# Kernel tuning notes

Measured on AMD Instinct MI355X. Metric: run time of the kernel, lower is better.

Reference implementation:

```python
import jax, jax.numpy as jnp
import numpy as np

N_NOTE = 14  # undefined global in original; must equal output_size for one-hot feedback


def setup_inputs() -> dict:
    key = jax.random.key(0)
    ks = jax.random.split(key, 9)
    B, T, H, O = 256, 512, 2048, 14
    s_i = 1.0 / np.sqrt(14)
    s_h = 1.0 / np.sqrt(H)
    return {
        "encoder_outputs": jax.random.normal(ks[0], (B, 1, H), jnp.float32),
        "encoder_hidden": jax.random.normal(ks[1], (1, B, H), jnp.float32),
        "target_tensor": jax.random.uniform(ks[2], (B, T, O), jnp.float32),
        "W_ih": jax.random.normal(ks[3], (3 * H, 14), jnp.float32) * s_i,
        "W_hh": jax.random.normal(ks[4], (3 * H, H), jnp.float32) * s_h,
        "b_ih": jax.random.normal(ks[5], (3 * H,), jnp.float32) * s_h,
        "b_hh": jax.random.normal(ks[6], (3 * H,), jnp.float32) * s_h,
        "W_out": jax.random.normal(ks[7], (O, H), jnp.float32) * s_h,
        "b_out": jax.random.normal(ks[8], (O,), jnp.float32) * s_h,
    }


def _decode(encoder_hidden, target_tensor, W_ih, W_hh, b_ih, b_hh, W_out, b_out):
    B, T, O = target_tensor.shape
    H = W_hh.shape[1]

    def step(carry, _):
        h, x = carry  # h: [B,H], x: [B,14]
        xr = jax.nn.relu(x)
        gi = xr @ W_ih.T + b_ih            # [B,3H]
        gh = h @ W_hh.T + b_hh             # [B,3H]
        r = jax.nn.sigmoid(gi[:, :H] + gh[:, :H])
        z = jax.nn.sigmoid(gi[:, H:2 * H] + gh[:, H:2 * H])
        n = jnp.tanh(gi[:, 2 * H:] + r * gh[:, 2 * H:])
        h_new = (1.0 - z) * n + z * h
        logits = h_new @ W_out.T + b_out   # [B,O]
        # feedback: one-hot of argmax; the Python `break` in the original zeros
        # every batch element at-or-after the first hit of n_note-1
        topi = jnp.argmax(logits, axis=-1)                     # [B]
        hit = (topi == N_NOTE - 1).astype(jnp.int32)
        alive = (jnp.cumsum(hit) == 0).astype(logits.dtype)    # inclusive cumsum
        x_next = jax.nn.one_hot(topi, O, dtype=logits.dtype) * alive[:, None]
        return (h_new, x_next), logits

    h0 = encoder_hidden[0]          # [B,H]
    x0 = target_tensor[:, 0]        # [B,14] first-step input
    (h_final, _), logits = jax.lax.scan(step, (h0, x0), None, length=T)
    logits = jnp.transpose(logits, (1, 0, 2))  # [B,T,O]
    log_probs = jax.nn.log_softmax(logits, axis=-1)
    return log_probs, h_final[None]  # ([B,T,O], [1,B,H])


def reference(encoder_outputs, encoder_hidden, target_tensor, W_ih, W_hh, b_ih, b_hh, W_out, b_out):
    # encoder_outputs is accepted but unused, matching the original forward
    return _decode(encoder_hidden, target_tensor, W_ih, W_hh, b_ih, b_hh, W_out, b_out)
```

## Files before the change

kernel.cpp:

```cpp
#include <hip/hip_runtime.h>
#include <math.h>

typedef float f4 __attribute__((ext_vector_type(4)));
typedef _Float16 f16x8 __attribute__((ext_vector_type(8)));
typedef _Float16 f16x4 __attribute__((ext_vector_type(4)));
typedef int i4 __attribute__((ext_vector_type(4)));

#define Hdim 2048
#define Bdim 256
#define Tdim 512
#define Odim 14
#define G3   6144


__global__ void prep_gtable(const float* __restrict__ b_ih,
                            const float* __restrict__ W_ih,
                            float* __restrict__ Gt) {
    int idx = blockIdx.x * 256 + threadIdx.x;
    if (idx >= 15 * G3) return;
    int c = idx / G3, row = idx % G3;
    float v = b_ih[row];
    if (c < Odim) v += W_ih[row * Odim + c];
    Gt[idx] = v;
}

__global__ void prep_gi0(const float* __restrict__ b_ih,
                         const float* __restrict__ W_ih,
                         const float* __restrict__ target,
                         float* __restrict__ gi0) {
    int idx = blockIdx.x * 256 + threadIdx.x;
    int b = idx / G3, row = idx % G3;
    const float* x0 = target + (size_t)b * (Tdim * Odim);
    float s = b_ih[row];
    #pragma unroll
    for (int c = 0; c < Odim; ++c)
        s = fmaf(fmaxf(x0[c], 0.f), W_ih[row * Odim + c], s);
    gi0[idx] = s;
}

__global__ void prep_Bpack(const float* __restrict__ W,
                           _Float16* __restrict__ Bh, _Float16* __restrict__ Bl) {
    int idx = blockIdx.x * 256 + threadIdx.x;
    int n = idx >> 8, kc = idx & 255;
    const float* src = W + (size_t)n * Hdim + kc * 8;
    int kb = kc >> 2, q = kc & 3;
    int lane = (n & 15) + 16 * q;
    int nt = n >> 4;
    f16x8 vh, vl;
    #pragma unroll
    for (int j = 0; j < 8; ++j) {
        float w = src[j];
        _Float16 h = (_Float16)w;
        vh[j] = h;
        vl[j] = (_Float16)(w - (float)h);
    }
    size_t off = (((size_t)nt * 64 + kb) * 64 + lane) * 8;
    *(f16x8*)(Bh + off) = vh;
    *(f16x8*)(Bl + off) = vl;
}

__global__ void prep_A0(const float* __restrict__ h0,
                        _Float16* __restrict__ Ah, _Float16* __restrict__ Al) {
    int idx = blockIdx.x * 256 + threadIdx.x;
    int m = idx >> 8, kc = idx & 255;
    const float* src = h0 + (size_t)m * Hdim + kc * 8;
    int kb = kc >> 2, q = kc & 3;
    int lane = (m & 15) + 16 * q;
    int mt = m >> 4;
    f16x8 vh, vl;
    #pragma unroll
    for (int j = 0; j < 8; ++j) {
        float w = src[j];
        _Float16 h = (_Float16)w;
        vh[j] = h;
        vl[j] = (_Float16)(w - (float)h);
    }
    size_t off = (((size_t)mt * 64 + kb) * 64 + lane) * 8;
    *(f16x8*)(Ah + off) = vh;
    *(f16x8*)(Al + off) = vl;
}

__global__ __launch_bounds__(512, 4)
void gemm_step(const _Float16* __restrict__ Ah, const _Float16* __restrict__ Al,
               const _Float16* __restrict__ Bh, const _Float16* __restrict__ Bl,
               float* __restrict__ Cpart) {
    __shared__ __align__(16) _Float16 sB[2][12288];

    const int tid = threadIdx.x;
    const int wave = tid >> 6, lane = tid & 63;
    const int nt0 = blockIdx.x * 3;
    const int kb0 = blockIdx.y * 16;

    f4 acc[2][3];
    #pragma unroll
    for (int mf = 0; mf < 2; ++mf)
        #pragma unroll
        for (int nf = 0; nf < 3; ++nf) acc[mf][nf] = (f4)0.f;

    auto stage = [&](int buf, int c) {
        #pragma unroll
        for (int i = 0; i < 3; ++i) {
            int e = i * 512 + tid;
            int half = (e >= 768) ? 1 : 0;
            int r = e - half * 768;
            int blk = r >> 6, l = e & 63;
            int ntl = blk >> 2, kbl = blk & 3;
            const _Float16* src = (half ? Bl : Bh) +
                ((((size_t)(nt0 + ntl) * 64) + kb0 + c * 4 + kbl) * 512 + l * 8);
            __builtin_amdgcn_global_load_lds(
                (const __attribute__((address_space(1))) void*)src,
                (__attribute__((address_space(3))) void*)(&sB[buf][(size_t)e * 8]),
                16, 0, 0);
        }
    };

    stage(0, 0);
    __syncthreads();

    for (int c = 0; c < 4; ++c) {
        const int buf = c & 1;
        if (c < 3) stage(buf ^ 1, c + 1);
        #pragma unroll
        for (int kbl = 0; kbl < 4; ++kbl) {
            const int kb = kb0 + c * 4 + kbl;
            f16x8 a_h[2], a_l[2], b_h[3], b_l[3];
            #pragma unroll
            for (int mf = 0; mf < 2; ++mf) {
                size_t off = (((size_t)(wave * 2 + mf) * 64 + kb) * 64 + lane) * 8;
                a_h[mf] = *(const f16x8*)(Ah + off);
                a_l[mf] = *(const f16x8*)(Al + off);
            }
            #pragma unroll
            for (int nf = 0; nf < 3; ++nf) {
                int base = ((nf * 4 + kbl) * 64 + lane) * 8;
                b_h[nf] = *(const f16x8*)(&sB[buf][base]);
                b_l[nf] = *(const f16x8*)(&sB[buf][6144 + base]);
            }
            #pragma unroll
            for (int mf = 0; mf < 2; ++mf)
                #pragma unroll
                for (int nf = 0; nf < 3; ++nf) {
                    acc[mf][nf] = __builtin_amdgcn_mfma_f32_16x16x32_f16(
                        a_h[mf], b_h[nf], acc[mf][nf], 0, 0, 0);
                    acc[mf][nf] = __builtin_amdgcn_mfma_f32_16x16x32_f16(
                        a_h[mf], b_l[nf], acc[mf][nf], 0, 0, 0);
                    acc[mf][nf] = __builtin_amdgcn_mfma_f32_16x16x32_f16(
                        a_l[mf], b_h[nf], acc[mf][nf], 0, 0, 0);
                }
        }
        __syncthreads();
    }

    const size_t base = (size_t)blockIdx.y * Bdim * G3;
    #pragma unroll
    for (int mf = 0; mf < 2; ++mf) {
        int mrow = wave * 32 + mf * 16 + (lane >> 4) * 4;
        #pragma unroll
        for (int nf = 0; nf < 3; ++nf) {
            int n = (nt0 + nf) * 16 + (lane & 15);
            #pragma unroll
            for (int q = 0; q < 4; ++q)
                Cpart[base + (size_t)(mrow + q) * G3 + n] = acc[mf][nf][q];
        }
    }
}

__global__ __launch_bounds__(512)
void fused_out(const float* __restrict__ hprev, float* __restrict__ hnew,
               const float* __restrict__ Cpart, const float* __restrict__ Gt,
               const float* __restrict__ gi0, const float* __restrict__ b_hh,
               const float* __restrict__ W_out, const float* __restrict__ b_out,
               _Float16* __restrict__ Ah, _Float16* __restrict__ Al,
               const int* __restrict__ topi_in, int* __restrict__ topi_out,
               float* __restrict__ lp, float* __restrict__ hfin, int t) {
    const int b = blockIdx.x;
    const int tid = threadIdx.x;
    __shared__ __align__(16) float sh[Hdim];
    __shared__ float sl[16];
    __shared__ int s_sel;
    __shared__ unsigned long long s_m[4];

    if (t > 0) {
        if (tid < 256) {
            int tp = topi_in[tid];
            unsigned long long m = __ballot(tp == (Odim - 1));
            if ((tid & 63) == 0) s_m[tid >> 6] = m;
        }
        __syncthreads();
        if (tid == 0) {
            int bw = b >> 6, bl = b & 63;
            unsigned long long le =
                s_m[bw] & ((bl == 63) ? ~0ULL : ((1ULL << (bl + 1)) - 1ULL));
            bool dead = (le != 0ULL);
            for (int w = 0; w < bw; ++w) dead = dead || (s_m[w] != 0ULL);
            s_sel = dead ? Odim : topi_in[b];
        }
        __syncthreads();
    }
    const float* gp = (t == 0) ? (gi0 + (size_t)b * G3)
                               : (Gt + (size_t)s_sel * G3);

    const int j0 = tid * 4;
    float hn[4];
    {
        float gsum[3][4];
        #pragma unroll
        for (int g = 0; g < 3; ++g) {
            f4 s = *(const f4*)(b_hh + g * Hdim + j0);
            #pragma unroll
            for (int ks = 0; ks < 4; ++ks)
                s += *(const f4*)(Cpart + ((size_t)ks * Bdim + b) * G3 + g * Hdim + j0);
            #pragma unroll
            for (int c = 0; c < 4; ++c) gsum[g][c] = s[c];
        }
        f4 hp = *(const f4*)(hprev + (size_t)b * Hdim + j0);
        f4 gr = *(const f4*)(gp + j0);
        f4 gz = *(const f4*)(gp + Hdim + j0);
        f4 gn = *(const f4*)(gp + 2 * Hdim + j0);
        #pragma unroll
        for (int c = 0; c < 4; ++c) {
            float rr = 1.f / (1.f + expf(-(gr[c] + gsum[0][c])));
            float zz = 1.f / (1.f + expf(-(gz[c] + gsum[1][c])));
            float nn = tanhf(fmaf(rr, gsum[2][c], gn[c]));
            hn[c] = (1.f - zz) * nn + zz * hp[c];
        }
    }
    f4 o0;
    #pragma unroll
    for (int c = 0; c < 4; ++c) o0[c] = hn[c];
    *(f4*)(hnew + (size_t)b * Hdim + j0) = o0;
    {
        f16x4 vh, vl;
        #pragma unroll
        for (int c = 0; c < 4; ++c) {
            _Float16 hh = (_Float16)hn[c];
            vh[c] = hh;
            vl[c] = (_Float16)(hn[c] - (float)hh);
        }
        int kb = j0 >> 5, q = (j0 >> 3) & 3, e0 = j0 & 7;
        int lane = (b & 15) + 16 * q, mt = b >> 4;
        size_t off = (((size_t)mt * 64 + kb) * 64 + lane) * 8 + e0;
        *(f16x4*)(Ah + off) = vh;
        *(f16x4*)(Al + off) = vl;
    }
    *(f4*)(sh + j0) = o0;
    __syncthreads();

    const int w = tid >> 6, l = tid & 63;
    for (int o = w; o < Odim; o += 8) {
        const float* wo = W_out + (size_t)o * Hdim;
        float s = 0.f;
        #pragma unroll
        for (int i = 0; i < 32; ++i)
            s = fmaf(sh[l + 64 * i], wo[l + 64 * i], s);
        #pragma unroll
        for (int off = 32; off >= 1; off >>= 1)
            s += __shfl_down(s, off);
        if (l == 0) sl[o] = s + b_out[o];
    }
    __syncthreads();
    if (tid == 0) {
        float m = sl[0]; int bi = 0;
        #pragma unroll
        for (int o = 1; o < Odim; ++o)
            if (sl[o] > m) { m = sl[o]; bi = o; }
        float ssum = 0.f;
        #pragma unroll
        for (int o = 0; o < Odim; ++o) ssum += expf(sl[o] - m);
        topi_out[b] = bi;
        sl[14] = m + logf(ssum);
    }
    __syncthreads();
    if (tid < Odim)
        lp[(size_t)b * (Tdim * Odim) + (size_t)t * Odim + tid] = sl[tid] - sl[14];
    if (hfin)
        *(f4*)(hfin + (size_t)b * Hdim + j0) = o0;
}

extern "C" void kernel_launch(void* const* d_in, const int* in_sizes, int n_in,
                              void* d_out, int out_size, void* d_ws, size_t ws_size,
                              hipStream_t stream) {
    const float* enc_hidden = (const float*)d_in[1];
    const float* target     = (const float*)d_in[2];
    const float* W_ih       = (const float*)d_in[3];
    const float* W_hh       = (const float*)d_in[4];
    const float* b_ih       = (const float*)d_in[5];
    const float* b_hh       = (const float*)d_in[6];
    const float* W_out      = (const float*)d_in[7];
    const float* b_out      = (const float*)d_in[8];

    float* out  = (float*)d_out;
    float* lp   = out;
    float* hfin = out + (size_t)Bdim * Tdim * Odim;

    float* ws    = (float*)d_ws;
    float* hb0   = ws;
    float* hb1   = hb0 + 524288;
    float* Gt    = hb1 + 524288;
    float* gi0   = Gt + 15 * G3;
    float* Cpart = gi0 + (size_t)Bdim * G3;
    _Float16* Ah = (_Float16*)(Cpart + 4 * (size_t)Bdim * G3);
    _Float16* Al = Ah + (size_t)Bdim * Hdim;
    _Float16* Bh = Al + (size_t)Bdim * Hdim;
    _Float16* Bl = Bh + (size_t)G3 * Hdim;
    int* topibuf = (int*)(Bl + (size_t)G3 * Hdim);

    prep_gtable<<<(15 * G3 + 255) / 256, 256, 0, stream>>>(b_ih, W_ih, Gt);
    prep_gi0<<<(Bdim * G3) / 256, 256, 0, stream>>>(b_ih, W_ih, target, gi0);
    prep_Bpack<<<(G3 * 256) / 256, 256, 0, stream>>>(W_hh, Bh, Bl);
    prep_A0<<<(Bdim * 256) / 256, 256, 0, stream>>>(enc_hidden, Ah, Al);

    for (int t = 0; t < Tdim; ++t) {
        float* hnew = (t & 1) ? hb1 : hb0;
        const float* hprev = (t == 0) ? enc_hidden : ((t & 1) ? hb0 : hb1);
        int* tin  = topibuf + ((t + 1) & 1) * 256;
        int* tout = topibuf + (t & 1) * 256;
        gemm_step<<<dim3(128, 4), 512, 0, stream>>>(Ah, Al, Bh, Bl, Cpart);
        fused_out<<<256, 512, 0, stream>>>(hprev, hnew, Cpart, Gt, gi0, b_hh,
                                           W_out, b_out, Ah, Al, tin, tout, lp,
                                           (t == Tdim - 1) ? hfin : nullptr, t);
    }
}
```

Baseline: 18.87 ms.

## Switch per-step GEMM to 32x32x16 MFMA tiles with larger block tiles

```diff
diff --git a/kernel.cpp b/kernel.cpp
--- a/kernel.cpp
+++ b/kernel.cpp
@@ -2,6 +2,7 @@
 #include <math.h>
 
 typedef float f4 __attribute__((ext_vector_type(4)));
+typedef float f16f __attribute__((ext_vector_type(16)));
 typedef _Float16 f16x8 __attribute__((ext_vector_type(8)));
 typedef _Float16 f16x4 __attribute__((ext_vector_type(4)));
 typedef int i4 __attribute__((ext_vector_type(4)));
@@ -43,9 +44,9 @@
     int idx = blockIdx.x * 256 + threadIdx.x;
     int n = idx >> 8, kc = idx & 255;
     const float* src = W + (size_t)n * Hdim + kc * 8;
-    int kb = kc >> 2, q = kc & 3;
-    int lane = (n & 15) + 16 * q;
-    int nt = n >> 4;
+    int kb = kc >> 1;
+    int lane = (n & 31) + 32 * (kc & 1);
+    int nt = n >> 5;
     f16x8 vh, vl;
     #pragma unroll
     for (int j = 0; j < 8; ++j) {
@@ -54,7 +55,7 @@
         vh[j] = h;
         vl[j] = (_Float16)(w - (float)h);
     }
-    size_t off = (((size_t)nt * 64 + kb) * 64 + lane) * 8;
+    size_t off = (((size_t)nt * 128 + kb) * 64 + lane) * 8;
     *(f16x8*)(Bh + off) = vh;
     *(f16x8*)(Bl + off) = vl;
 }
@@ -64,9 +65,9 @@
     int idx = blockIdx.x * 256 + threadIdx.x;
     int m = idx >> 8, kc = idx & 255;
     const float* src = h0 + (size_t)m * Hdim + kc * 8;
-    int kb = kc >> 2, q = kc & 3;
-    int lane = (m & 15) + 16 * q;
-    int mt = m >> 4;
+    int kb = kc >> 1;
+    int lane = (m & 31) + 32 * (kc & 1);
+    int mt = m >> 5;
     f16x8 vh, vl;
     #pragma unroll
     for (int j = 0; j < 8; ++j) {
@@ -75,38 +76,41 @@
         vh[j] = h;
         vl[j] = (_Float16)(w - (float)h);
     }
-    size_t off = (((size_t)mt * 64 + kb) * 64 + lane) * 8;
+    size_t off = (((size_t)mt * 128 + kb) * 64 + lane) * 8;
     *(f16x8*)(Ah + off) = vh;
     *(f16x8*)(Al + off) = vl;
 }
 
-__global__ __launch_bounds__(512, 4)
+__global__ __launch_bounds__(256, 1)
 void gemm_step(const _Float16* __restrict__ Ah, const _Float16* __restrict__ Al,
                const _Float16* __restrict__ Bh, const _Float16* __restrict__ Bl,
                float* __restrict__ Cpart) {
-    __shared__ __align__(16) _Float16 sB[2][12288];
+    __shared__ __align__(16) _Float16 sB[2][24576];
 
     const int tid = threadIdx.x;
     const int wave = tid >> 6, lane = tid & 63;
-    const int nt0 = blockIdx.x * 3;
-    const int kb0 = blockIdx.y * 16;
-
-    f4 acc[2][3];
+    const int Mg = wave & 1;
+    const int Ng = wave >> 1;
+    const int mb = blockIdx.x & 1;
+    const int nb = blockIdx.x >> 1;
+    const int kb0 = blockIdx.y * 32;
+
+    f16f acc[2][3];
     #pragma unroll
     for (int mf = 0; mf < 2; ++mf)
         #pragma unroll
-        for (int nf = 0; nf < 3; ++nf) acc[mf][nf] = (f4)0.f;
+        for (int nf = 0; nf < 3; ++nf) acc[mf][nf] = (f16f)0.f;
 
     auto stage = [&](int buf, int c) {
         #pragma unroll
-        for (int i = 0; i < 3; ++i) {
-            int e = i * 512 + tid;
-            int half = (e >= 768) ? 1 : 0;
-            int r = e - half * 768;
+        for (int i = 0; i < 12; ++i) {
+            int e = i * 256 + tid;
+            int half = (e >= 1536) ? 1 : 0;
+            int r = e - half * 1536;
             int blk = r >> 6, l = e & 63;
-            int ntl = blk >> 2, kbl = blk & 3;
+            int ntl = blk >> 2, kl = blk & 3;
             const _Float16* src = (half ? Bl : Bh) +
-                ((((size_t)(nt0 + ntl) * 64) + kb0 + c * 4 + kbl) * 512 + l * 8);
+                ((((size_t)(nb * 6 + ntl) * 128) + kb0 + c * 4 + kl) * 512 + l * 8);
             __builtin_amdgcn_global_load_lds(
                 (const __attribute__((address_space(1))) void*)src,
                 (__attribute__((address_space(3))) void*)(&sB[buf][(size_t)e * 8]),
@@ -117,34 +121,35 @@
     stage(0, 0);
     __syncthreads();
 
-    for (int c = 0; c < 4; ++c) {
+    for (int c = 0; c < 8; ++c) {
         const int buf = c & 1;
-        if (c < 3) stage(buf ^ 1, c + 1);
-        #pragma unroll
-        for (int kbl = 0; kbl < 4; ++kbl) {
-            const int kb = kb0 + c * 4 + kbl;
+        if (c < 7) stage(buf ^ 1, c + 1);
+        #pragma unroll
+        for (int kl = 0; kl < 4; ++kl) {
+            const int kb = kb0 + c * 4 + kl;
             f16x8 a_h[2], a_l[2], b_h[3], b_l[3];
             #pragma unroll
             for (int mf = 0; mf < 2; ++mf) {
-                size_t off = (((size_t)(wave * 2 + mf) * 64 + kb) * 64 + lane) * 8;
+                int mt = mb * 4 + Mg * 2 + mf;
+                size_t off = (((size_t)mt * 128 + kb) * 64 + lane) * 8;
                 a_h[mf] = *(const f16x8*)(Ah + off);
                 a_l[mf] = *(const f16x8*)(Al + off);
             }
             #pragma unroll
             for (int nf = 0; nf < 3; ++nf) {
-                int base = ((nf * 4 + kbl) * 64 + lane) * 8;
+                int base = (((Ng * 3 + nf) * 4 + kl) * 64 + lane) * 8;
                 b_h[nf] = *(const f16x8*)(&sB[buf][base]);
-                b_l[nf] = *(const f16x8*)(&sB[buf][6144 + base]);
+                b_l[nf] = *(const f16x8*)(&sB[buf][12288 + base]);
             }
             #pragma unroll
             for (int mf = 0; mf < 2; ++mf)
                 #pragma unroll
                 for (int nf = 0; nf < 3; ++nf) {
-                    acc[mf][nf] = __builtin_amdgcn_mfma_f32_16x16x32_f16(
+                    acc[mf][nf] = __builtin_amdgcn_mfma_f32_32x32x16_f16(
                         a_h[mf], b_h[nf], acc[mf][nf], 0, 0, 0);
-                    acc[mf][nf] = __builtin_amdgcn_mfma_f32_16x16x32_f16(
+                    acc[mf][nf] = __builtin_amdgcn_mfma_f32_32x32x16_f16(
                         a_h[mf], b_l[nf], acc[mf][nf], 0, 0, 0);
-                    acc[mf][nf] = __builtin_amdgcn_mfma_f32_16x16x32_f16(
+                    acc[mf][nf] = __builtin_amdgcn_mfma_f32_32x32x16_f16(
                         a_l[mf], b_h[nf], acc[mf][nf], 0, 0, 0);
                 }
         }
@@ -152,15 +157,18 @@
     }
 
     const size_t base = (size_t)blockIdx.y * Bdim * G3;
+    const int rbase = 4 * (lane >> 5);
     #pragma unroll
     for (int mf = 0; mf < 2; ++mf) {
-        int mrow = wave * 32 + mf * 16 + (lane >> 4) * 4;
+        int m0 = mb * 128 + Mg * 64 + mf * 32 + rbase;
         #pragma unroll
         for (int nf = 0; nf < 3; ++nf) {
-            int n = (nt0 + nf) * 16 + (lane & 15);
+            int n = nb * 192 + (Ng * 3 + nf) * 32 + (lane & 31);
             #pragma unroll
-            for (int q = 0; q < 4; ++q)
-                Cpart[base + (size_t)(mrow + q) * G3 + n] = acc[mf][nf][q];
+            for (int q = 0; q < 16; ++q) {
+                int m = m0 + (q & 3) + 8 * (q >> 2);
+                Cpart[base + (size_t)m * G3 + n] = acc[mf][nf][q];
+            }
         }
     }
 }
@@ -180,6 +188,20 @@
     __shared__ int s_sel;
     __shared__ unsigned long long s_m[4];
 
+    const int j0 = tid * 4;
+
+    float gsum[3][4];
+    #pragma unroll
+    for (int g = 0; g < 3; ++g) {
+        f4 s = *(const f4*)(b_hh + g * Hdim + j0);
+        #pragma unroll
+        for (int ks = 0; ks < 4; ++ks)
+            s += *(const f4*)(Cpart + ((size_t)ks * Bdim + b) * G3 + g * Hdim + j0);
+        #pragma unroll
+        for (int c = 0; c < 4; ++c) gsum[g][c] = s[c];
+    }
+    f4 hp = *(const f4*)(hprev + (size_t)b * Hdim + j0);
+
     if (t > 0) {
         if (tid < 256) {
             int tp = topi_in[tid];
@@ -200,20 +222,8 @@
     const float* gp = (t == 0) ? (gi0 + (size_t)b * G3)
                                : (Gt + (size_t)s_sel * G3);
 
-    const int j0 = tid * 4;
     float hn[4];
     {
-        float gsum[3][4];
-        #pragma unroll
-        for (int g = 0; g < 3; ++g) {
-            f4 s = *(const f4*)(b_hh + g * Hdim + j0);
-            #pragma unroll
-            for (int ks = 0; ks < 4; ++ks)
-                s += *(const f4*)(Cpart + ((size_t)ks * Bdim + b) * G3 + g * Hdim + j0);
-            #pragma unroll
-            for (int c = 0; c < 4; ++c) gsum[g][c] = s[c];
-        }
-        f4 hp = *(const f4*)(hprev + (size_t)b * Hdim + j0);
         f4 gr = *(const f4*)(gp + j0);
         f4 gz = *(const f4*)(gp + Hdim + j0);
         f4 gn = *(const f4*)(gp + 2 * Hdim + j0);
@@ -237,9 +247,9 @@
             vh[c] = hh;
             vl[c] = (_Float16)(hn[c] - (float)hh);
         }
-        int kb = j0 >> 5, q = (j0 >> 3) & 3, e0 = j0 & 7;
-        int lane = (b & 15) + 16 * q, mt = b >> 4;
-        size_t off = (((size_t)mt * 64 + kb) * 64 + lane) * 8 + e0;
+        int kb = j0 >> 4, half = (j0 >> 3) & 1, e0 = j0 & 7;
+        int lane = (b & 31) + 32 * half, mt = b >> 5;
+        size_t off = (((size_t)mt * 128 + kb) * 64 + lane) * 8 + e0;
         *(f16x4*)(Ah + off) = vh;
         *(f16x4*)(Al + off) = vl;
     }
@@ -315,7 +325,7 @@
         const float* hprev = (t == 0) ? enc_hidden : ((t & 1) ? hb0 : hb1);
         int* tin  = topibuf + ((t + 1) & 1) * 256;
         int* tout = topibuf + (t & 1) * 256;
-        gemm_step<<<dim3(128, 4), 512, 0, stream>>>(Ah, Al, Bh, Bl, Cpart);
+        gemm_step<<<dim3(64, 4), 256, 0, stream>>>(Ah, Al, Bh, Bl, Cpart);
         fused_out<<<256, 512, 0, stream>>>(hprev, hnew, Cpart, Gt, gi0, b_hh,
                                            W_out, b_out, Ah, Al, tin, tout, lp,
                                            (t == Tdim - 1) ? hfin : nullptr, t);
```

Result: slower. 22.27 ms (+18.0%).

## Fuse GRU gate epilogue into GEMM with in-block split-K reduction

Applied to the files above, without the earlier changes.

```diff
diff --git a/kernel.cpp b/kernel.cpp
--- a/kernel.cpp
+++ b/kernel.cpp
@@ -3,8 +3,6 @@
 
 typedef float f4 __attribute__((ext_vector_type(4)));
 typedef _Float16 f16x8 __attribute__((ext_vector_type(8)));
-typedef _Float16 f16x4 __attribute__((ext_vector_type(4)));
-typedef int i4 __attribute__((ext_vector_type(4)));
 
 #define Hdim 2048
 #define Bdim 256
@@ -80,16 +78,32 @@
     *(f16x8*)(Al + off) = vl;
 }
 
-__global__ __launch_bounds__(512, 4)
-void gemm_step(const _Float16* __restrict__ Ah, const _Float16* __restrict__ Al,
-               const _Float16* __restrict__ Bh, const _Float16* __restrict__ Bl,
-               float* __restrict__ Cpart) {
-    __shared__ __align__(16) _Float16 sB[2][12288];
+__global__ __launch_bounds__(512, 2)
+void gru_step(const _Float16* __restrict__ Aih, const _Float16* __restrict__ Ail,
+              const _Float16* __restrict__ Bh, const _Float16* __restrict__ Bl,
+              const float* __restrict__ hprev, float* __restrict__ hnew,
+              const float* __restrict__ Gt, const float* __restrict__ gi0,
+              const float* __restrict__ b_hh,
+              const int* __restrict__ topi_in,
+              _Float16* __restrict__ Aoh, _Float16* __restrict__ Aol,
+              int t) {
+    __shared__ __align__(16) _Float16 sB[2][24576];
+    __shared__ unsigned long long s_m[4];
+    __shared__ int s_tp[256];
 
     const int tid = threadIdx.x;
     const int wave = tid >> 6, lane = tid & 63;
-    const int nt0 = blockIdx.x * 3;
-    const int kb0 = blockIdx.y * 16;
+    const int Mg = wave & 3;
+    const int kg = wave >> 2;
+    const int mb = blockIdx.x & 1;
+    const int nb = blockIdx.x >> 1;
+
+    if (t > 0 && tid < 256) {
+        int tp = topi_in[tid];
+        s_tp[tid] = tp;
+        unsigned long long mk = __ballot(tp == (Odim - 1));
+        if (lane == 0) s_m[tid >> 6] = mk;
+    }
 
     f4 acc[2][3];
     #pragma unroll
@@ -99,14 +113,17 @@
 
     auto stage = [&](int buf, int c) {
         #pragma unroll
-        for (int i = 0; i < 3; ++i) {
+        for (int i = 0; i < 6; ++i) {
             int e = i * 512 + tid;
-            int half = (e >= 768) ? 1 : 0;
-            int r = e - half * 768;
-            int blk = r >> 6, l = e & 63;
+            int ekg = (e >= 1536) ? 1 : 0;
+            int r = e - ekg * 1536;
+            int half = (r >= 768) ? 1 : 0;
+            int r2 = r - half * 768;
+            int blk = r2 >> 6, l = e & 63;
             int ntl = blk >> 2, kbl = blk & 3;
-            const _Float16* src = (half ? Bl : Bh) +
-                ((((size_t)(nt0 + ntl) * 64) + kb0 + c * 4 + kbl) * 512 + l * 8);
+            int kb = ekg * 32 + c * 4 + kbl;
+            size_t nt = (size_t)ntl * 128 + nb;
+            const _Float16* src = (half ? Bl : Bh) + ((nt * 64 + kb) * 64 + l) * 8;
             __builtin_amdgcn_global_load_lds(
                 (const __attribute__((address_space(1))) void*)src,
                 (__attribute__((address_space(3))) void*)(&sB[buf][(size_t)e * 8]),
@@ -117,22 +134,24 @@
     stage(0, 0);
     __syncthreads();
 
-    for (int c = 0; c < 4; ++c) {
+    const int kbase = kg * 12288;
+    for (int c = 0; c < 8; ++c) {
         const int buf = c & 1;
-        if (c < 3) stage(buf ^ 1, c + 1);
-        #pragma unroll
-        for (int kbl = 0; kbl < 4; ++kbl) {
-            const int kb = kb0 + c * 4 + kbl;
+        if (c < 7) stage(buf ^ 1, c + 1);
+        #pragma unroll
+        for (int kl = 0; kl < 4; ++kl) {
+            const int kb = kg * 32 + c * 4 + kl;
             f16x8 a_h[2], a_l[2], b_h[3], b_l[3];
             #pragma unroll
             for (int mf = 0; mf < 2; ++mf) {
-                size_t off = (((size_t)(wave * 2 + mf) * 64 + kb) * 64 + lane) * 8;
-                a_h[mf] = *(const f16x8*)(Ah + off);
-                a_l[mf] = *(const f16x8*)(Al + off);
+                int mt = mb * 8 + Mg * 2 + mf;
+                size_t off = (((size_t)mt * 64 + kb) * 64 + lane) * 8;
+                a_h[mf] = *(const f16x8*)(Aih + off);
+                a_l[mf] = *(const f16x8*)(Ail + off);
             }
             #pragma unroll
             for (int nf = 0; nf < 3; ++nf) {
-                int base = ((nf * 4 + kbl) * 64 + lane) * 8;
+                int base = kbase + ((nf * 4 + kl) * 64 + lane) * 8;
                 b_h[nf] = *(const f16x8*)(&sB[buf][base]);
                 b_l[nf] = *(const f16x8*)(&sB[buf][6144 + base]);
             }
@@ -151,98 +170,76 @@
         __syncthreads();
     }
 
-    const size_t base = (size_t)blockIdx.y * Bdim * G3;
-    #pragma unroll
-    for (int mf = 0; mf < 2; ++mf) {
-        int mrow = wave * 32 + mf * 16 + (lane >> 4) * 4;
-        #pragma unroll
-        for (int nf = 0; nf < 3; ++nf) {
-            int n = (nt0 + nf) * 16 + (lane & 15);
-            #pragma unroll
-            for (int q = 0; q < 4; ++q)
-                Cpart[base + (size_t)(mrow + q) * G3 + n] = acc[mf][nf][q];
+    float* red = (float*)sB;
+    if (kg == 1) {
+        #pragma unroll
+        for (int mf = 0; mf < 2; ++mf)
+            #pragma unroll
+            for (int nf = 0; nf < 3; ++nf)
+                *(f4*)&red[(((Mg * 64 + lane) * 6) + mf * 3 + nf) * 4] = acc[mf][nf];
+    }
+    __syncthreads();
+    if (kg == 0) {
+        #pragma unroll
+        for (int mf = 0; mf < 2; ++mf)
+            #pragma unroll
+            for (int nf = 0; nf < 3; ++nf)
+                acc[mf][nf] += *(const f4*)&red[(((Mg * 64 + lane) * 6) + mf * 3 + nf) * 4];
+
+        const int col = nb * 16 + (lane & 15);
+        const float bhr = b_hh[col];
+        const float bhz = b_hh[Hdim + col];
+        const float bhn = b_hh[2 * Hdim + col];
+        #pragma unroll
+        for (int mf = 0; mf < 2; ++mf) {
+            #pragma unroll
+            for (int q = 0; q < 4; ++q) {
+                int m = mb * 128 + Mg * 32 + mf * 16 + ((lane >> 4) << 2) + q;
+                float gr, gz, gn;
+                if (t == 0) {
+                    const float* g = gi0 + (size_t)m * G3;
+                    gr = g[col]; gz = g[Hdim + col]; gn = g[2 * Hdim + col];
+                } else {
+                    int bw = m >> 6, bl = m & 63;
+                    unsigned long long le =
+                        s_m[bw] & ((bl == 63) ? ~0ULL : ((1ULL << (bl + 1)) - 1ULL));
+                    bool dead = (le != 0ULL);
+                    if (bw > 0) dead = dead || (s_m[0] != 0ULL);
+                    if (bw > 1) dead = dead || (s_m[1] != 0ULL);
+                    if (bw > 2) dead = dead || (s_m[2] != 0ULL);
+                    int sel = dead ? Odim : s_tp[m];
+                    const float* g = Gt + (size_t)sel * G3;
+                    gr = g[col]; gz = g[Hdim + col]; gn = g[2 * Hdim + col];
+                }
+                float hp = hprev[(size_t)m * Hdim + col];
+                float rr = 1.f / (1.f + expf(-(gr + (acc[mf][0][q] + bhr))));
+                float zz = 1.f / (1.f + expf(-(gz + (acc[mf][1][q] + bhz))));
+                float nn = tanhf(fmaf(rr, acc[mf][2][q] + bhn, gn));
+                float hv = (1.f - zz) * nn + zz * hp;
+                hnew[(size_t)m * Hdim + col] = hv;
+                _Float16 hh = (_Float16)hv;
+                int kb2 = col >> 5, q2 = (col >> 3) & 3, e0 = col & 7;
+                int lane2 = (m & 15) + 16 * q2, mt2 = m >> 4;
+                size_t aoff = (((size_t)mt2 * 64 + kb2) * 64 + lane2) * 8 + e0;
+                Aoh[aoff] = hh;
+                Aol[aoff] = (_Float16)(hv - (float)hh);
+            }
         }
     }
 }
 
 __global__ __launch_bounds__(512)
-void fused_out(const float* __restrict__ hprev, float* __restrict__ hnew,
-               const float* __restrict__ Cpart, const float* __restrict__ Gt,
-               const float* __restrict__ gi0, const float* __restrict__ b_hh,
-               const float* __restrict__ W_out, const float* __restrict__ b_out,
-               _Float16* __restrict__ Ah, _Float16* __restrict__ Al,
-               const int* __restrict__ topi_in, int* __restrict__ topi_out,
-               float* __restrict__ lp, float* __restrict__ hfin, int t) {
+void logits_out(const float* __restrict__ hnew,
+                const float* __restrict__ W_out, const float* __restrict__ b_out,
+                int* __restrict__ topi_out, float* __restrict__ lp,
+                float* __restrict__ hfin, int t) {
     const int b = blockIdx.x;
     const int tid = threadIdx.x;
     __shared__ __align__(16) float sh[Hdim];
     __shared__ float sl[16];
-    __shared__ int s_sel;
-    __shared__ unsigned long long s_m[4];
-
-    if (t > 0) {
-        if (tid < 256) {
-            int tp = topi_in[tid];
-            unsigned long long m = __ballot(tp == (Odim - 1));
-            if ((tid & 63) == 0) s_m[tid >> 6] = m;
-        }
-        __syncthreads();
-        if (tid == 0) {
-            int bw = b >> 6, bl = b & 63;
-            unsigned long long le =
-                s_m[bw] & ((bl == 63) ? ~0ULL : ((1ULL << (bl + 1)) - 1ULL));
-            bool dead = (le != 0ULL);
-            for (int w = 0; w < bw; ++w) dead = dead || (s_m[w] != 0ULL);
-            s_sel = dead ? Odim : topi_in[b];
-        }
-        __syncthreads();
-    }
-    const float* gp = (t == 0) ? (gi0 + (size_t)b * G3)
-                               : (Gt + (size_t)s_sel * G3);
 
     const int j0 = tid * 4;
-    float hn[4];
-    {
-        float gsum[3][4];
-        #pragma unroll
-        for (int g = 0; g < 3; ++g) {
-            f4 s = *(const f4*)(b_hh + g * Hdim + j0);
-            #pragma unroll
-            for (int ks = 0; ks < 4; ++ks)
-                s += *(const f4*)(Cpart + ((size_t)ks * Bdim + b) * G3 + g * Hdim + j0);
-            #pragma unroll
-            for (int c = 0; c < 4; ++c) gsum[g][c] = s[c];
-        }
-        f4 hp = *(const f4*)(hprev + (size_t)b * Hdim + j0);
-        f4 gr = *(const f4*)(gp + j0);
-        f4 gz = *(const f4*)(gp + Hdim + j0);
-        f4 gn = *(const f4*)(gp + 2 * Hdim + j0);
-        #pragma unroll
-        for (int c = 0; c < 4; ++c) {
-            float rr = 1.f / (1.f + expf(-(gr[c] + gsum[0][c])));
-            float zz = 1.f / (1.f + expf(-(gz[c] + gsum[1][c])));
-            float nn = tanhf(fmaf(rr, gsum[2][c], gn[c]));
-            hn[c] = (1.f - zz) * nn + zz * hp[c];
-        }
-    }
-    f4 o0;
-    #pragma unroll
-    for (int c = 0; c < 4; ++c) o0[c] = hn[c];
-    *(f4*)(hnew + (size_t)b * Hdim + j0) = o0;
-    {
-        f16x4 vh, vl;
-        #pragma unroll
-        for (int c = 0; c < 4; ++c) {
-            _Float16 hh = (_Float16)hn[c];
-            vh[c] = hh;
-            vl[c] = (_Float16)(hn[c] - (float)hh);
-        }
-        int kb = j0 >> 5, q = (j0 >> 3) & 3, e0 = j0 & 7;
-        int lane = (b & 15) + 16 * q, mt = b >> 4;
-        size_t off = (((size_t)mt * 64 + kb) * 64 + lane) * 8 + e0;
-        *(f16x4*)(Ah + off) = vh;
-        *(f16x4*)(Al + off) = vl;
-    }
+    f4 o0 = *(const f4*)(hnew + (size_t)b * Hdim + j0);
     *(f4*)(sh + j0) = o0;
     __syncthreads();
 
@@ -298,26 +295,32 @@
     float* hb1   = hb0 + 524288;
     float* Gt    = hb1 + 524288;
     float* gi0   = Gt + 15 * G3;
-    float* Cpart = gi0 + (size_t)Bdim * G3;
-    _Float16* Ah = (_Float16*)(Cpart + 4 * (size_t)Bdim * G3);
-    _Float16* Al = Ah + (size_t)Bdim * Hdim;
-    _Float16* Bh = Al + (size_t)Bdim * Hdim;
+    float* apad  = gi0 + (size_t)Bdim * G3;
+    _Float16* A0h = (_Float16*)apad;
+    _Float16* A0l = A0h + (size_t)Bdim * Hdim;
+    _Float16* A1h = A0l + (size_t)Bdim * Hdim;
+    _Float16* A1l = A1h + (size_t)Bdim * Hdim;
+    _Float16* Bh = (_Float16*)(apad + 4 * (size_t)Bdim * G3);
     _Float16* Bl = Bh + (size_t)G3 * Hdim;
     int* topibuf = (int*)(Bl + (size_t)G3 * Hdim);
 
     prep_gtable<<<(15 * G3 + 255) / 256, 256, 0, stream>>>(b_ih, W_ih, Gt);
     prep_gi0<<<(Bdim * G3) / 256, 256, 0, stream>>>(b_ih, W_ih, target, gi0);
     prep_Bpack<<<(G3 * 256) / 256, 256, 0, stream>>>(W_hh, Bh, Bl);
-    prep_A0<<<(Bdim * 256) / 256, 256, 0, stream>>>(enc_hidden, Ah, Al);
+    prep_A0<<<(Bdim * 256) / 256, 256, 0, stream>>>(enc_hidden, A0h, A0l);
 
     for (int t = 0; t < Tdim; ++t) {
         float* hnew = (t & 1) ? hb1 : hb0;
         const float* hprev = (t == 0) ? enc_hidden : ((t & 1) ? hb0 : hb1);
+        const _Float16* Aih = (t & 1) ? A1h : A0h;
+        const _Float16* Ail = (t & 1) ? A1l : A0l;
+        _Float16* Aoh = (t & 1) ? A0h : A1h;
+        _Float16* Aol = (t & 1) ? A0l : A1l;
         int* tin  = topibuf + ((t + 1) & 1) * 256;
         int* tout = topibuf + (t & 1) * 256;
-        gemm_step<<<dim3(128, 4), 512, 0, stream>>>(Ah, Al, Bh, Bl, Cpart);
-        fused_out<<<256, 512, 0, stream>>>(hprev, hnew, Cpart, Gt, gi0, b_hh,
-                                           W_out, b_out, Ah, Al, tin, tout, lp,
-                                           (t == Tdim - 1) ? hfin : nullptr, t);
-    }
-}
+        gru_step<<<256, 512, 0, stream>>>(Aih, Ail, Bh, Bl, hprev, hnew,
+                                          Gt, gi0, b_hh, tin, Aoh, Aol, t);
+        logits_out<<<256, 512, 0, stream>>>(hnew, W_out, b_out, tout, lp,
+                                            (t == Tdim - 1) ? hfin : nullptr, t);
+    }
+}
```

After: 23.69 ms. 1.26x slower.
